# Kernel optimization log

Hardware: AMD Instinct MI355X
Metric: run time of the kernel (lower is better)

Reference implementation:

```python
import jax, jax.numpy as jnp
import numpy as np


def setup_inputs() -> dict:
    key = jax.random.key(0)
    k1, k2 = jax.random.split(key)
    D, N, M = 256, 1024, 1024
    z_x = jax.random.normal(k1, (1, D, N), dtype=jnp.float32)
    z_y = jax.random.normal(k2, (1, D, M), dtype=jnp.float32)
    return {"z_x": z_x, "z_y": z_y}


def reference(z_x, z_y):
    # squeeze().t(): (1, d, N) -> (N, d)
    x = jnp.squeeze(z_x).T  # (N, d)
    y = jnp.squeeze(z_y).T  # (M, d)
    # L1 compare: s[i, j] = -sum_d |x[i, d] - y[j, d]|  -> (N, M)
    s = -jnp.sum(jnp.abs(x[:, None, :] - y[None, :, :]), axis=-1)
    a = jax.nn.softmax(s, axis=1)  # row-wise softmax
    b = jax.nn.softmax(s, axis=0)  # column-wise softmax
    a = a + b - a * b              # soft union of alignments
    return jnp.sum(a * s) / jnp.sum(a)
```

## Files before the change

### kernel.cpp

```cpp
#include <hip/hip_runtime.h>
#include <math.h>


#define DD 256
#define NN 1024
#define NQ 256

__device__ __forceinline__ float waveMax(float v) {
  #pragma unroll
  for (int off = 32; off; off >>= 1) v = fmaxf(v, __shfl_xor(v, off, 64));
  return v;
}
__device__ __forceinline__ float waveSum(float v) {
  #pragma unroll
  for (int off = 32; off; off >>= 1) v += __shfl_xor(v, off, 64);
  return v;
}


__global__ __launch_bounds__(256, 2)
void scompute_kernel(const float* __restrict__ zx, const float* __restrict__ zy,
                     float* __restrict__ S,
                     float* __restrict__ pRM, float* __restrict__ pRL,
                     float* __restrict__ pCM, float* __restrict__ pCL) {
  const int bx = blockIdx.x;
  const int by = blockIdx.y;
  const int i0 = by * 16;
  const int t  = threadIdx.x;
  const int w  = t >> 6;
  const int ln = t & 63;

  __shared__ float xs[DD][16];
  __shared__ float ys[2][8][128];
  __shared__ float cmS[4][128];
  __shared__ float clS[4][128];

  const float4* __restrict__ X4 = (const float4*)zx;
  const float4* __restrict__ Y4 = (const float4*)zy;

  #pragma unroll
  for (int i = 0; i < 4; ++i) {
    const int k = t + i * 256;
    const int d = k >> 2, rq = k & 3;
    *(float4*)&xs[d][rq * 4] = X4[d * NQ + by * 4 + rq];
  }

  const int sd = t >> 5;
  const int sq = t & 31;
  const int jq0 = bx * 32;
  *(float4*)&ys[0][sd][sq * 4] = Y4[sd * NQ + jq0 + sq];
  __syncthreads();

  float acc[4][2];
  #pragma unroll
  for (int r = 0; r < 4; ++r) { acc[r][0] = 0.f; acc[r][1] = 0.f; }

  #pragma unroll 1
  for (int n = 0; n < DD / 8; ++n) {
    const int buf = n & 1;
    float4 p0;
    if (n < DD / 8 - 1)
      p0 = Y4[(8 * (n + 1) + sd) * NQ + jq0 + sq];
    #pragma unroll
    for (int dd = 0; dd < 8; ++dd) {
      const int d = n * 8 + dd;
      const float4 xv = *(const float4*)&xs[d][w * 4];
      const float2 yv = *(const float2*)&ys[buf][dd][ln * 2];
      acc[0][0] += fabsf(xv.x - yv.x); acc[0][1] += fabsf(xv.x - yv.y);
      acc[1][0] += fabsf(xv.y - yv.x); acc[1][1] += fabsf(xv.y - yv.y);
      acc[2][0] += fabsf(xv.z - yv.x); acc[2][1] += fabsf(xv.z - yv.y);
      acc[3][0] += fabsf(xv.w - yv.x); acc[3][1] += fabsf(xv.w - yv.y);
    }
    if (n < DD / 8 - 1)
      *(float4*)&ys[buf ^ 1][sd][sq * 4] = p0;
    __syncthreads();
  }

  float2* __restrict__ S2 = (float2*)S;
  #pragma unroll
  for (int r = 0; r < 4; ++r)
    S2[(i0 + w * 4 + r) * (NN / 2) + bx * 64 + ln] = make_float2(acc[r][0], acc[r][1]);

  #pragma unroll
  for (int r = 0; r < 4; ++r) {
    float m = fmaxf(-acc[r][0], -acc[r][1]);
    m = waveMax(m);
    float l = __expf(-acc[r][0] - m) + __expf(-acc[r][1] - m);
    l = waveSum(l);
    if (ln == 0) {
      pRM[bx * NN + i0 + w * 4 + r] = m;
      pRL[bx * NN + i0 + w * 4 + r] = l;
    }
  }

  #pragma unroll
  for (int c = 0; c < 2; ++c) {
    float m = fmaxf(fmaxf(-acc[0][c], -acc[1][c]), fmaxf(-acc[2][c], -acc[3][c]));
    float l = __expf(-acc[0][c] - m) + __expf(-acc[1][c] - m) +
              __expf(-acc[2][c] - m) + __expf(-acc[3][c] - m);
    cmS[w][ln * 2 + c] = m;
    clS[w][ln * 2 + c] = l;
  }
  __syncthreads();
  if (t < 128) {
    const int j = t;
    const float m0 = cmS[0][j], m1 = cmS[1][j], m2 = cmS[2][j], m3 = cmS[3][j];
    const float M = fmaxf(fmaxf(m0, m1), fmaxf(m2, m3));
    const float L = clS[0][j] * __expf(m0 - M) + clS[1][j] * __expf(m1 - M) +
                    clS[2][j] * __expf(m2 - M) + clS[3][j] * __expf(m3 - M);
    pCM[by * NN + bx * 128 + j] = M;
    pCL[by * NN + bx * 128 + j] = L;
  }
}

__global__ __launch_bounds__(256)
void combine_kernel(const float* __restrict__ pRM, const float* __restrict__ pRL,
                    const float* __restrict__ pCM, const float* __restrict__ pCL,
                    float* __restrict__ rmax, float* __restrict__ rsum,
                    float* __restrict__ cmax, float* __restrict__ csum,
                    float* __restrict__ accum) {
  const int b = blockIdx.x, t = threadIdx.x;
  if (b == 0 && t == 0) {
    accum[0] = 0.f; accum[1] = 0.f; ((unsigned int*)accum)[2] = 0u;
  }
  if (b < 4) {
    const int r = b * 256 + t;
    float mk[8], lk[8];
    #pragma unroll
    for (int k = 0; k < 8; ++k) { mk[k] = pRM[k * NN + r]; lk[k] = pRL[k * NN + r]; }
    float m = mk[0];
    #pragma unroll
    for (int k = 1; k < 8; ++k) m = fmaxf(m, mk[k]);
    float l = 0.f;
    #pragma unroll
    for (int k = 0; k < 8; ++k) l += lk[k] * __expf(mk[k] - m);
    rmax[r] = m; rsum[r] = l;
  } else {
    const int j = (b - 4) * 256 + t;
    float m = -1e30f;
    #pragma unroll 8
    for (int k = 0; k < 64; ++k) m = fmaxf(m, pCM[k * NN + j]);
    float l = 0.f;
    #pragma unroll 8
    for (int k = 0; k < 64; ++k) l += __expf(pCM[k * NN + j] - m) * pCL[k * NN + j];
    cmax[j] = m; csum[j] = l;
  }
}

__global__ __launch_bounds__(256)
void final_kernel(const float* __restrict__ S,
                  const float* __restrict__ rmax, const float* __restrict__ rsum,
                  const float* __restrict__ cmax, const float* __restrict__ csum,
                  float* __restrict__ accum, float* __restrict__ out) {
  __shared__ float redn[4], redd[4];
  const int t = threadIdx.x;
  const int row0 = blockIdx.x * 2;
  const float4* S4 = (const float4*)S;
  const float4 cm = ((const float4*)cmax)[t];
  const float4 cs = ((const float4*)csum)[t];
  float un = 0.f, ud = 0.f;
  #pragma unroll
  for (int r = 0; r < 2; ++r) {
    const int row = row0 + r;
    const float rm = rmax[row];
    const float ri = 1.f / rsum[row];
    const float4 p = S4[row * NQ + t];
    {
      const float s = -p.x;
      const float a = __expf(s - rm) * ri;
      const float b = __expf(s - cm.x) / cs.x;
      const float u = a + b - a * b;
      un += u * s; ud += u;
    }
    {
      const float s = -p.y;
      const float a = __expf(s - rm) * ri;
      const float b = __expf(s - cm.y) / cs.y;
      const float u = a + b - a * b;
      un += u * s; ud += u;
    }
    {
      const float s = -p.z;
      const float a = __expf(s - rm) * ri;
      const float b = __expf(s - cm.z) / cs.z;
      const float u = a + b - a * b;
      un += u * s; ud += u;
    }
    {
      const float s = -p.w;
      const float a = __expf(s - rm) * ri;
      const float b = __expf(s - cm.w) / cs.w;
      const float u = a + b - a * b;
      un += u * s; ud += u;
    }
  }
  un = waveSum(un); ud = waveSum(ud);
  if ((t & 63) == 0) { redn[t >> 6] = un; redd[t >> 6] = ud; }
  __syncthreads();
  if (t == 0) {
    atomicAdd(&accum[0], redn[0] + redn[1] + redn[2] + redn[3]);
    atomicAdd(&accum[1], redd[0] + redd[1] + redd[2] + redd[3]);
    __threadfence();
    unsigned int* cnt = (unsigned int*)accum + 2;
    const unsigned int old = atomicAdd(cnt, 1u);
    if (old == gridDim.x - 1) {
      const float n = atomicAdd(&accum[0], 0.f);
      const float d = atomicAdd(&accum[1], 0.f);
      out[0] = n / d;
    }
  }
}


#define TJ  128
#define NCH (NN / TJ)
#define BLK 256

__global__ __launch_bounds__(BLK)
void stats2_kernel(const float* __restrict__ zx, const float* __restrict__ zy,
                   float* __restrict__ partM, float* __restrict__ partS) {
  const int side = blockIdx.z;
  const float* __restrict__ X = side ? zy : zx;
  const float* __restrict__ Y = side ? zx : zy;
  const int j0 = blockIdx.x * TJ;
  const int i0 = blockIdx.y * 8;
  const int t  = threadIdx.x;
  const int rg = t >> 5;
  const int c  = t & 31;

  __shared__ float xs[8 * DD];
  for (int k = t; k < 8 * DD; k += BLK)
    xs[k] = X[(k >> 3) * NN + i0 + (k & 7)];
  __syncthreads();

  const float4* __restrict__ Y4 = (const float4*)Y;
  const int yb = (j0 >> 2) + c;
  float4 acc = make_float4(0.f, 0.f, 0.f, 0.f);
  #pragma unroll 8
  for (int d = 0; d < DD; ++d) {
    const float4 yv = Y4[d * NQ + yb];
    const float xv = xs[d * 8 + rg];
    acc.x += fabsf(xv - yv.x);
    acc.y += fabsf(xv - yv.y);
    acc.z += fabsf(xv - yv.z);
    acc.w += fabsf(xv - yv.w);
  }

  float m = fmaxf(fmaxf(-acc.x, -acc.y), fmaxf(-acc.z, -acc.w));
  #pragma unroll
  for (int off = 16; off > 0; off >>= 1) m = fmaxf(m, __shfl_xor(m, off, 32));
  float p = __expf(-acc.x - m) + __expf(-acc.y - m) +
            __expf(-acc.z - m) + __expf(-acc.w - m);
  #pragma unroll
  for (int off = 16; off > 0; off >>= 1) p += __shfl_xor(p, off, 32);

  if (c == 0) {
    const int idx = side * (NCH * NN) + blockIdx.x * NN + (i0 + rg);
    partM[idx] = m;
    partS[idx] = p;
  }
}

__global__ __launch_bounds__(BLK)
void combine_kernel_fb(const float* __restrict__ partM, const float* __restrict__ partS,
                       float* __restrict__ rmax, float* __restrict__ rsum,
                       float* __restrict__ cmax, float* __restrict__ csum,
                       float* __restrict__ accum) {
  const int gid = blockIdx.x * BLK + threadIdx.x;
  if (gid == 0) { accum[0] = 0.f; accum[1] = 0.f; }
  const int sd = gid >> 10;
  const int i  = gid & (NN - 1);
  float mk[NCH], sk[NCH];
  #pragma unroll
  for (int k = 0; k < NCH; ++k) {
    mk[k] = partM[sd * (NCH * NN) + k * NN + i];
    sk[k] = partS[sd * (NCH * NN) + k * NN + i];
  }
  float m = mk[0];
  #pragma unroll
  for (int k = 1; k < NCH; ++k) m = fmaxf(m, mk[k]);
  float s = 0.f;
  #pragma unroll
  for (int k = 0; k < NCH; ++k) s += __expf(mk[k] - m) * sk[k];
  if (sd == 0) { rmax[i] = m; rsum[i] = s; }
  else         { cmax[i] = m; csum[i] = s; }
}

__global__ __launch_bounds__(BLK)
void final2_kernel(const float* __restrict__ zx, const float* __restrict__ zy,
                   const float* __restrict__ rmax, const float* __restrict__ rsum,
                   const float* __restrict__ cmax, const float* __restrict__ csum,
                   float* __restrict__ accum) {
  const int j0 = blockIdx.x * TJ;
  const int i0 = blockIdx.y * 8;
  const int t  = threadIdx.x;
  const int rg = t >> 5;
  const int c  = t & 31;

  __shared__ float xs[8 * DD];
  __shared__ float redn[4], redd[4];
  for (int k = t; k < 8 * DD; k += BLK)
    xs[k] = zx[(k >> 3) * NN + i0 + (k & 7)];
  __syncthreads();

  const float4* __restrict__ Y4 = (const float4*)zy;
  const int yb = (j0 >> 2) + c;
  float4 acc = make_float4(0.f, 0.f, 0.f, 0.f);
  #pragma unroll 8
  for (int d = 0; d < DD; ++d) {
    const float4 yv = Y4[d * NQ + yb];
    const float xv = xs[d * 8 + rg];
    acc.x += fabsf(xv - yv.x);
    acc.y += fabsf(xv - yv.y);
    acc.z += fabsf(xv - yv.z);
    acc.w += fabsf(xv - yv.w);
  }

  const int i = i0 + rg;
  const float rm = rmax[i];
  const float ri = 1.f / rsum[i];
  const float4 cm = ((const float4*)cmax)[yb];
  const float4 cs = ((const float4*)csum)[yb];

  float un = 0.f, ud = 0.f;
  {
    const float s = -acc.x;
    const float a = __expf(s - rm) * ri;
    const float b = __expf(s - cm.x) / cs.x;
    const float u = a + b - a * b;
    un += u * s; ud += u;
  }
  {
    const float s = -acc.y;
    const float a = __expf(s - rm) * ri;
    const float b = __expf(s - cm.y) / cs.y;
    const float u = a + b - a * b;
    un += u * s; ud += u;
  }
  {
    const float s = -acc.z;
    const float a = __expf(s - rm) * ri;
    const float b = __expf(s - cm.z) / cs.z;
    const float u = a + b - a * b;
    un += u * s; ud += u;
  }
  {
    const float s = -acc.w;
    const float a = __expf(s - rm) * ri;
    const float b = __expf(s - cm.w) / cs.w;
    const float u = a + b - a * b;
    un += u * s; ud += u;
  }

  un = waveSum(un); ud = waveSum(ud);
  if ((t & 63) == 0) { redn[t >> 6] = un; redd[t >> 6] = ud; }
  __syncthreads();
  if (t == 0) {
    atomicAdd(&accum[0], redn[0] + redn[1] + redn[2] + redn[3]);
    atomicAdd(&accum[1], redd[0] + redd[1] + redd[2] + redd[3]);
  }
}

__global__ void finalize_kernel(const float* __restrict__ accum, float* __restrict__ out) {
  out[0] = accum[0] / accum[1];
}


extern "C" void kernel_launch(void* const* d_in, const int* in_sizes, int n_in,
                              void* d_out, int out_size, void* d_ws, size_t ws_size,
                              hipStream_t stream) {
  const float* zx = (const float*)d_in[0];
  const float* zy = (const float*)d_in[1];
  float* ws  = (float*)d_ws;
  float* out = (float*)d_out;

  float* accum = ws;
  float* S     = ws + 16;
  float* pRM   = S + NN * NN;
  float* pRL   = pRM + 8 * NN;
  float* pCM   = pRL + 8 * NN;
  float* pCL   = pCM + 64 * NN;
  float* rmax  = pCL + 64 * NN;
  float* rsum  = rmax + NN;
  float* cmax  = rsum + NN;
  float* csum  = cmax + NN;
  const size_t need = (size_t)((csum + NN) - ws) * sizeof(float);

  if (ws_size >= need) {
    dim3 g1(8, 64);
    scompute_kernel<<<g1, 256, 0, stream>>>(zx, zy, S, pRM, pRL, pCM, pCL);
    combine_kernel<<<8, 256, 0, stream>>>(pRM, pRL, pCM, pCL,
                                          rmax, rsum, cmax, csum, accum);
    final_kernel<<<NN / 2, 256, 0, stream>>>(S, rmax, rsum, cmax, csum, accum, out);
  } else {
    float* partM = ws + 16;
    float* partS = partM + 2 * NCH * NN;
    float* frmax = partS + 2 * NCH * NN;
    float* frsum = frmax + NN;
    float* fcmax = frsum + NN;
    float* fcsum = fcmax + NN;
    dim3 sgrid(NCH, NN / 8, 2);
    stats2_kernel<<<sgrid, BLK, 0, stream>>>(zx, zy, partM, partS);
    combine_kernel_fb<<<(2 * NN) / BLK, BLK, 0, stream>>>(partM, partS,
                                                          frmax, frsum, fcmax, fcsum, accum);
    dim3 fgrid(NCH, NN / 8);
    final2_kernel<<<fgrid, BLK, 0, stream>>>(zx, zy, frmax, frsum, fcmax, fcsum, accum);
    finalize_kernel<<<1, 1, 0, stream>>>(accum, out);
  }
}
```

Before: 121.1 us.

## Double y-tile depth per stage and parallelize column combine across more blocks

The main kernel now stages 16 feature rows of y per double-buffered step instead of 8. This halves the number of loop iterations and __syncthreads barriers, at the cost of more LDS and two prefetch loads per thread. The combine kernel splits each column's 64-partial reduction across four wave groups in 16 blocks, with an LDS merge. This replaces 4 blocks doing serial 64-long loops and is meant to shorten the latency of the small combine launch.

```diff
diff --git a/kernel.cpp b/kernel.cpp
--- a/kernel.cpp
+++ b/kernel.cpp
@@ -31,7 +31,7 @@
   const int ln = t & 63;
 
   __shared__ float xs[DD][16];
-  __shared__ float ys[2][8][128];
+  __shared__ float ys[2][16][128];
   __shared__ float cmS[4][128];
   __shared__ float clS[4][128];
 
@@ -45,10 +45,11 @@
     *(float4*)&xs[d][rq * 4] = X4[d * NQ + by * 4 + rq];
   }
 
-  const int sd = t >> 5;
-  const int sq = t & 31;
+  const int sd = t >> 4;
+  const int sq = t & 15;
   const int jq0 = bx * 32;
-  *(float4*)&ys[0][sd][sq * 4] = Y4[sd * NQ + jq0 + sq];
+  *(float4*)&ys[0][sd][sq * 4]        = Y4[sd * NQ + jq0 + sq];
+  *(float4*)&ys[0][sd][(sq + 16) * 4] = Y4[sd * NQ + jq0 + sq + 16];
   __syncthreads();
 
   float acc[4][2];
@@ -56,14 +57,16 @@
   for (int r = 0; r < 4; ++r) { acc[r][0] = 0.f; acc[r][1] = 0.f; }
 
   #pragma unroll 1
-  for (int n = 0; n < DD / 8; ++n) {
+  for (int n = 0; n < DD / 16; ++n) {
     const int buf = n & 1;
-    float4 p0;
-    if (n < DD / 8 - 1)
-      p0 = Y4[(8 * (n + 1) + sd) * NQ + jq0 + sq];
-    #pragma unroll
-    for (int dd = 0; dd < 8; ++dd) {
-      const int d = n * 8 + dd;
+    float4 p0, p1;
+    if (n < DD / 16 - 1) {
+      p0 = Y4[(16 * (n + 1) + sd) * NQ + jq0 + sq];
+      p1 = Y4[(16 * (n + 1) + sd) * NQ + jq0 + sq + 16];
+    }
+    #pragma unroll
+    for (int dd = 0; dd < 16; ++dd) {
+      const int d = n * 16 + dd;
       const float4 xv = *(const float4*)&xs[d][w * 4];
       const float2 yv = *(const float2*)&ys[buf][dd][ln * 2];
       acc[0][0] += fabsf(xv.x - yv.x); acc[0][1] += fabsf(xv.x - yv.y);
@@ -71,8 +74,10 @@
       acc[2][0] += fabsf(xv.z - yv.x); acc[2][1] += fabsf(xv.z - yv.y);
       acc[3][0] += fabsf(xv.w - yv.x); acc[3][1] += fabsf(xv.w - yv.y);
     }
-    if (n < DD / 8 - 1)
-      *(float4*)&ys[buf ^ 1][sd][sq * 4] = p0;
+    if (n < DD / 16 - 1) {
+      *(float4*)&ys[buf ^ 1][sd][sq * 4]        = p0;
+      *(float4*)&ys[buf ^ 1][sd][(sq + 16) * 4] = p1;
+    }
     __syncthreads();
   }
 
@@ -123,8 +128,29 @@
   if (b == 0 && t == 0) {
     accum[0] = 0.f; accum[1] = 0.f; ((unsigned int*)accum)[2] = 0u;
   }
-  if (b < 4) {
-    const int r = b * 256 + t;
+  if (b < 16) {
+    __shared__ float sm[4][64], sl[4][64];
+    const int c = t & 63;
+    const int g = t >> 6;
+    const int j = b * 64 + c;
+    float m = -1e30f;
+    #pragma unroll
+    for (int k = 0; k < 16; ++k) m = fmaxf(m, pCM[(g * 16 + k) * NN + j]);
+    float l = 0.f;
+    #pragma unroll
+    for (int k = 0; k < 16; ++k)
+      l += __expf(pCM[(g * 16 + k) * NN + j] - m) * pCL[(g * 16 + k) * NN + j];
+    sm[g][c] = m; sl[g][c] = l;
+    __syncthreads();
+    if (g == 0) {
+      const float m0 = sm[0][c], m1 = sm[1][c], m2 = sm[2][c], m3 = sm[3][c];
+      const float M = fmaxf(fmaxf(m0, m1), fmaxf(m2, m3));
+      const float L = sl[0][c] * __expf(m0 - M) + sl[1][c] * __expf(m1 - M) +
+                      sl[2][c] * __expf(m2 - M) + sl[3][c] * __expf(m3 - M);
+      cmax[j] = M; csum[j] = L;
+    }
+  } else {
+    const int r = (b - 16) * 256 + t;
     float mk[8], lk[8];
     #pragma unroll
     for (int k = 0; k < 8; ++k) { mk[k] = pRM[k * NN + r]; lk[k] = pRL[k * NN + r]; }
@@ -135,15 +161,6 @@
     #pragma unroll
     for (int k = 0; k < 8; ++k) l += lk[k] * __expf(mk[k] - m);
     rmax[r] = m; rsum[r] = l;
-  } else {
-    const int j = (b - 4) * 256 + t;
-    float m = -1e30f;
-    #pragma unroll 8
-    for (int k = 0; k < 64; ++k) m = fmaxf(m, pCM[k * NN + j]);
-    float l = 0.f;
-    #pragma unroll 8
-    for (int k = 0; k < 64; ++k) l += __expf(pCM[k * NN + j] - m) * pCL[k * NN + j];
-    cmax[j] = m; csum[j] = l;
   }
 }
 
@@ -389,8 +406,8 @@
   if (ws_size >= need) {
     dim3 g1(8, 64);
     scompute_kernel<<<g1, 256, 0, stream>>>(zx, zy, S, pRM, pRL, pCM, pCL);
-    combine_kernel<<<8, 256, 0, stream>>>(pRM, pRL, pCM, pCL,
-                                          rmax, rsum, cmax, csum, accum);
+    combine_kernel<<<20, 256, 0, stream>>>(pRM, pRL, pCM, pCL,
+                                           rmax, rsum, cmax, csum, accum);
     final_kernel<<<NN / 2, 256, 0, stream>>>(S, rmax, rsum, cmax, csum, accum, out);
   } else {
     float* partM = ws + 16;
```

Result: faster. 105.5 us (-12.8%).
